# Performance work log

Hardware: AMD Instinct MI355X
Metric: run time of the kernel (lower is better)

Reference implementation:

```python
import jax, jax.numpy as jnp
import numpy as np

B, TV, TS, D = 16, 256, 32, 512


def setup_inputs() -> dict:
    key = jax.random.key(0)
    ks = jax.random.split(key, 8)
    return {
        "video_feature": jax.random.normal(ks[0], (B, TV, D), dtype=jnp.float32),
        "video_mask": jnp.ones((B, TV), dtype=jnp.float32),
        "sentence_feature": jax.random.normal(ks[1], (B, TS, D), dtype=jnp.float32),
        "sentence_mask": jnp.ones((B, TS), dtype=jnp.float32),
        "w1": jax.random.normal(ks[2], (D, D), dtype=jnp.float32) * (1.0 / np.sqrt(D)),
        "b1": jax.random.normal(ks[3], (D,), dtype=jnp.float32) * 0.02,
        "w2": jax.random.normal(ks[4], (D, D), dtype=jnp.float32) * (1.0 / np.sqrt(D)),
        "wt": jax.random.normal(ks[5], (D,), dtype=jnp.float32) * (1.0 / np.sqrt(D)),
    }


def reference(video_feature, video_mask, sentence_feature, sentence_mask, w1, b1, w2, wt):
    # tmp1: [B, Tv, D] masked video projection (Linear with bias)
    tmp1 = (jnp.einsum("bvd,ed->bve", video_feature, w1) + b1) * video_mask[:, :, None]
    # tmp2: [B, Ts, D] masked sentence projection (Linear, no bias)
    tmp2 = jnp.einsum("bsd,ed->bse", sentence_feature, w2) * sentence_mask[:, :, None]
    # pairwise mask: [B, Tv, Ts]
    pair_mask = video_mask[:, :, None] * sentence_mask[:, None, :]
    # broadcast-add -> [B, Tv, Ts, D], mask, tanh, reduce with wt -> [B, Tv, Ts]
    tmp = (tmp1[:, :, None, :] + tmp2[:, None, :, :]) * pair_mask[..., None]
    M = jnp.einsum("bvsd,d->bvs", jnp.tanh(tmp), wt)
    return M * pair_mask
```

## Files before the change

kernel.cpp:

```cpp
#include <hip/hip_runtime.h>

#define BB 16
#define TV 256
#define TS 32
#define DD 512

typedef float    floatx4  __attribute__((ext_vector_type(4)));
typedef short    short8   __attribute__((ext_vector_type(8)));
typedef unsigned short ushort8 __attribute__((ext_vector_type(8)));

static __device__ __forceinline__ unsigned short f2bf(float f) {
    unsigned int u = __float_as_uint(f);
    u += 0x7FFFu + ((u >> 16) & 1u);
    return (unsigned short)(u >> 16);
}

__global__ __launch_bounds__(256) void ta_convert(
    const float* __restrict__ video, const float* __restrict__ sent,
    const float* __restrict__ w1,    const float* __restrict__ w2,
    unsigned short* __restrict__ vb, unsigned short* __restrict__ sb,
    unsigned short* __restrict__ w1b, unsigned short* __restrict__ w2b)
{
    const int NV = BB * TV * DD, NS = BB * TS * DD, NW = DD * DD;
    const int base = (blockIdx.x * 256 + threadIdx.x) * 8;
    const float* src; unsigned short* dst; int off;
    if      (base < NV)           { src = video; dst = vb;  off = base; }
    else if (base < NV + NS)      { src = sent;  dst = sb;  off = base - NV; }
    else if (base < NV + NS + NW) { src = w1;    dst = w1b; off = base - NV - NS; }
    else                          { src = w2;    dst = w2b; off = base - NV - NS - NW; }
    const float4 a = *(const float4*)(src + off);
    const float4 b = *(const float4*)(src + off + 4);
    ushort8 o;
    o[0] = f2bf(a.x); o[1] = f2bf(a.y); o[2] = f2bf(a.z); o[3] = f2bf(a.w);
    o[4] = f2bf(b.x); o[5] = f2bf(b.y); o[6] = f2bf(b.z); o[7] = f2bf(b.w);
    *(ushort8*)(dst + off) = o;
}

__global__ __launch_bounds__(256) void ta_mfma_gemm(
    const unsigned short* __restrict__ vb, const unsigned short* __restrict__ w1b,
    const float* __restrict__ b1,          const float* __restrict__ vmask,
    float* __restrict__ tmp1,
    const unsigned short* __restrict__ sb, const unsigned short* __restrict__ w2b,
    const float* __restrict__ smask,       unsigned short* __restrict__ tmp2,
    const float* __restrict__ wt,          float* __restrict__ wsum)
{
    const int t = threadIdx.x;

    if (blockIdx.x == 0 && t < 64) {
        float v = 0.f;
        for (int i = t; i < DD; i += 64) v += wt[i];
        for (int off = 32; off; off >>= 1) v += __shfl_down(v, off);
        if (t == 0) wsum[0] = v;
    }

    const bool g2 = (blockIdx.x >= 512);
    const int bid = g2 ? (int)blockIdx.x - 512 : (int)blockIdx.x;
    const unsigned short* __restrict__ A  = g2 ? sb    : vb;
    const unsigned short* __restrict__ W  = g2 ? w2b   : w1b;
    const float* __restrict__ rm          = g2 ? smask : vmask;
    const int m0 = (bid >> 3) * 64;
    const int n0 = (bid & 7) * 64;

    __shared__ unsigned short As[64 * 64];
    __shared__ unsigned short Bs[64 * 64];

    const int lane = t & 63;
    const int wid  = t >> 6;
    const int wm   = wid >> 1, wn = wid & 1;
    const int lr   = lane & 15, kg = lane >> 4;

    const int row0 = t >> 3, c80 = t & 7;
    const int row1 = (t + 256) >> 3, c81 = t & 7;
    const int idx0 = row0 * 64 + ((c80 ^ (row0 & 7)) << 3);
    const int idx1 = row1 * 64 + ((c81 ^ (row1 & 7)) << 3);

    floatx4 acc[2][2] = {};

    for (int k0 = 0; k0 < DD; k0 += 64) {
        const ushort8 a0v = *(const ushort8*)&A[(size_t)(m0 + row0) * DD + k0 + c80 * 8];
        const ushort8 a1v = *(const ushort8*)&A[(size_t)(m0 + row1) * DD + k0 + c81 * 8];
        const ushort8 b0v = *(const ushort8*)&W[(size_t)(n0 + row0) * DD + k0 + c80 * 8];
        const ushort8 b1v = *(const ushort8*)&W[(size_t)(n0 + row1) * DD + k0 + c81 * 8];
        __syncthreads();
        *(ushort8*)&As[idx0] = a0v;
        *(ushort8*)&As[idx1] = a1v;
        *(ushort8*)&Bs[idx0] = b0v;
        *(ushort8*)&Bs[idx1] = b1v;
        __syncthreads();

#pragma unroll
        for (int kk = 0; kk < 2; ++kk) {
            const int kc = kk * 4 + kg;
            const int ml0 = wm * 32 + lr, ml1 = ml0 + 16;
            const int nl0 = wn * 32 + lr, nl1 = nl0 + 16;
            short8 a0 = *(const short8*)&As[ml0 * 64 + ((kc ^ (ml0 & 7)) << 3)];
            short8 a1 = *(const short8*)&As[ml1 * 64 + ((kc ^ (ml1 & 7)) << 3)];
            short8 b0 = *(const short8*)&Bs[nl0 * 64 + ((kc ^ (nl0 & 7)) << 3)];
            short8 b1 = *(const short8*)&Bs[nl1 * 64 + ((kc ^ (nl1 & 7)) << 3)];
            acc[0][0] = __builtin_amdgcn_mfma_f32_16x16x32_bf16(a0, b0, acc[0][0], 0, 0, 0);
            acc[0][1] = __builtin_amdgcn_mfma_f32_16x16x32_bf16(a0, b1, acc[0][1], 0, 0, 0);
            acc[1][0] = __builtin_amdgcn_mfma_f32_16x16x32_bf16(a1, b0, acc[1][0], 0, 0, 0);
            acc[1][1] = __builtin_amdgcn_mfma_f32_16x16x32_bf16(a1, b1, acc[1][1], 0, 0, 0);
        }
    }

#pragma unroll
    for (int fm = 0; fm < 2; ++fm)
#pragma unroll
        for (int fn = 0; fn < 2; ++fn)
#pragma unroll
            for (int r = 0; r < 4; ++r) {
                const int m = m0 + wm * 32 + fm * 16 + kg * 4 + r;
                const int n = n0 + wn * 32 + fn * 16 + lr;
                const float mk = rm[m];
                const float val = acc[fm][fn][r];
                if (!g2) tmp1[(size_t)m * DD + n] = (val + b1[n]) * mk;
                else     tmp2[(size_t)m * DD + n] = f2bf(val * mk);
            }
}

__global__ __launch_bounds__(512) void ta_tanh_main(
    const float* __restrict__ tmp1,
    const unsigned short* __restrict__ tmp2,
    const float* __restrict__ wt,
    const float* __restrict__ wsum,
    const float* __restrict__ vmask,
    const float* __restrict__ smask,
    float* __restrict__ out)
{
    __shared__ unsigned short t2s[TS * DD];
    __shared__ float part[512];

    const int t  = threadIdx.x;
    const int b  = blockIdx.x >> 6;
    const int v0 = (blockIdx.x & 63) << 2;

    {
        const unsigned short* src = tmp2 + (size_t)b * TS * DD;
#pragma unroll
        for (int i = 0; i < 4; ++i) {
            const int chunk = t + 512 * i;
            const int row = chunk >> 6;
            const int c   = chunk & 63;
            ushort8 val = *(const ushort8*)&src[chunk * 8];
            *(ushort8*)&t2s[row * DD + ((c ^ (row & 15)) << 3)] = val;
        }
    }
    __syncthreads();

    const int s  = t & 31;
    const int vi = (t >> 5) & 3;
    const int q  = __builtin_amdgcn_readfirstlane(t >> 7);
    const int v  = v0 + vi;

    const float pm = vmask[b * TV + v] * smask[b * TS + s];
    const float ce = pm * 2.885390082f;
    const float* __restrict__ x1p = tmp1 + ((size_t)(b * TV + v)) * DD + q * 128;
    const float* __restrict__ wtp = wt + q * 128;
    const int rowbase = s * DD;
    const int swz = s & 15;

    float acc0 = 0.f, acc1 = 0.f;
#pragma unroll 2
    for (int i = 0; i < 16; ++i) {
        ushort8 x2v = *(const ushort8*)&t2s[rowbase + (((q * 16 + i) ^ swz) << 3)];
        floatx4 x1a = *(const floatx4*)(x1p + i * 8);
        floatx4 x1b = *(const floatx4*)(x1p + i * 8 + 4);
#pragma unroll
        for (int j = 0; j < 4; ++j) {
            const float x2f = __uint_as_float((unsigned)x2v[j] << 16);
            const float e   = __builtin_amdgcn_exp2f((x1a[j] + x2f) * ce);
            acc0 = fmaf(wtp[i * 8 + j], __builtin_amdgcn_rcpf(e + 1.f), acc0);
        }
#pragma unroll
        for (int j = 0; j < 4; ++j) {
            const float x2f = __uint_as_float((unsigned)x2v[j + 4] << 16);
            const float e   = __builtin_amdgcn_exp2f((x1b[j] + x2f) * ce);
            acc1 = fmaf(wtp[i * 8 + j + 4], __builtin_amdgcn_rcpf(e + 1.f), acc1);
        }
    }

    part[t] = acc0 + acc1;
    __syncthreads();

    if (t < 128) {
        const float sum = part[t] + part[t + 128] + part[t + 256] + part[t + 384];
        const int s2 = t & 31, vi2 = t >> 5;
        const int v2 = v0 + vi2;
        const float pm2 = vmask[b * TV + v2] * smask[b * TS + s2];
        out[((size_t)b * TV + v2) * TS + s2] = pm2 * (wsum[0] - 2.f * sum);
    }
}

extern "C" void kernel_launch(void* const* d_in, const int* in_sizes, int n_in,
                              void* d_out, int out_size, void* d_ws, size_t ws_size,
                              hipStream_t stream)
{
    const float* video = (const float*)d_in[0];
    const float* vmask = (const float*)d_in[1];
    const float* sent  = (const float*)d_in[2];
    const float* smask = (const float*)d_in[3];
    const float* w1    = (const float*)d_in[4];
    const float* b1    = (const float*)d_in[5];
    const float* w2    = (const float*)d_in[6];
    const float* wt    = (const float*)d_in[7];
    float* out = (float*)d_out;

    const size_t NV = (size_t)BB * TV * DD, NS = (size_t)BB * TS * DD, NW = (size_t)DD * DD;

    float* tmp1          = (float*)d_ws;
    unsigned short* tmp2 = (unsigned short*)(tmp1 + NV);
    float* wsum          = (float*)(tmp2 + NS);
    unsigned short* vb   = (unsigned short*)(wsum + 4);
    unsigned short* sb   = vb + NV;
    unsigned short* w1b  = sb + NS;
    unsigned short* w2b  = w1b + NW;

    const int total8 = (int)((NV + NS + 2 * NW) / 8);
    ta_convert<<<dim3(total8 / 256), dim3(256), 0, stream>>>(
        video, sent, w1, w2, vb, sb, w1b, w2b);
    ta_mfma_gemm<<<dim3(512 + 64), dim3(256), 0, stream>>>(
        vb, w1b, b1, vmask, tmp1, sb, w2b, smask, tmp2, wt, wsum);
    ta_tanh_main<<<dim3(BB * (TV / 4)), dim3(512), 0, stream>>>(
        tmp1, tmp2, wt, wsum, vmask, smask, out);
}
```

Measured before the change: 42.58 us.

## Store tmp1 in bf16 and double-buffer GEMM with direct global-to-LDS loads

```diff
diff --git a/kernel.cpp b/kernel.cpp
--- a/kernel.cpp
+++ b/kernel.cpp
@@ -39,7 +39,7 @@
 __global__ __launch_bounds__(256) void ta_mfma_gemm(
     const unsigned short* __restrict__ vb, const unsigned short* __restrict__ w1b,
     const float* __restrict__ b1,          const float* __restrict__ vmask,
-    float* __restrict__ tmp1,
+    unsigned short* __restrict__ tmp1,
     const unsigned short* __restrict__ sb, const unsigned short* __restrict__ w2b,
     const float* __restrict__ smask,       unsigned short* __restrict__ tmp2,
     const float* __restrict__ wt,          float* __restrict__ wsum)
@@ -55,54 +55,74 @@
 
     const bool g2 = (blockIdx.x >= 512);
     const int bid = g2 ? (int)blockIdx.x - 512 : (int)blockIdx.x;
-    const unsigned short* __restrict__ A  = g2 ? sb    : vb;
-    const unsigned short* __restrict__ W  = g2 ? w2b   : w1b;
-    const float* __restrict__ rm          = g2 ? smask : vmask;
-    const int m0 = (bid >> 3) * 64;
-    const int n0 = (bid & 7) * 64;
-
-    __shared__ unsigned short As[64 * 64];
-    __shared__ unsigned short Bs[64 * 64];
+    const unsigned short* __restrict__ A = g2 ? sb    : vb;
+    const unsigned short* __restrict__ W = g2 ? w2b   : w1b;
+    const float* __restrict__ rm         = g2 ? smask : vmask;
+    const int m0 = (g2 ? (bid & 7)  : (bid & 63)) * 64;
+    const int n0 = (g2 ? (bid >> 3) : (bid >> 6)) * 64;
+
+    __shared__ unsigned short As[2][4096];
+    __shared__ unsigned short Bs[2][4096];
 
     const int lane = t & 63;
     const int wid  = t >> 6;
     const int wm   = wid >> 1, wn = wid & 1;
     const int lr   = lane & 15, kg = lane >> 4;
 
-    const int row0 = t >> 3, c80 = t & 7;
-    const int row1 = (t + 256) >> 3, c81 = t & 7;
-    const int idx0 = row0 * 64 + ((c80 ^ (row0 & 7)) << 3);
-    const int idx1 = row1 * 64 + ((c81 ^ (row1 & 7)) << 3);
+    const int r0 = t >> 3,          g0c = (t & 7) ^ (r0 & 7);
+    const int r1 = (t + 256) >> 3,  g1c = (t & 7) ^ (r1 & 7);
+    const unsigned short* a0p = A + (size_t)(m0 + r0) * DD + g0c * 8;
+    const unsigned short* a1p = A + (size_t)(m0 + r1) * DD + g1c * 8;
+    const unsigned short* w0p = W + (size_t)(n0 + r0) * DD + g0c * 8;
+    const unsigned short* w1p = W + (size_t)(n0 + r1) * DD + g1c * 8;
+    const int l0 = t * 8;
+    const int l1 = (t + 256) * 8;
+
+#define TA_STAGE(buf, koff) do {                                               \
+    __builtin_amdgcn_global_load_lds(                                          \
+        (const __attribute__((address_space(1))) void*)(a0p + (koff)),         \
+        (__attribute__((address_space(3))) void*)&As[buf][l0], 16, 0, 0);      \
+    __builtin_amdgcn_global_load_lds(                                          \
+        (const __attribute__((address_space(1))) void*)(a1p + (koff)),         \
+        (__attribute__((address_space(3))) void*)&As[buf][l1], 16, 0, 0);      \
+    __builtin_amdgcn_global_load_lds(                                          \
+        (const __attribute__((address_space(1))) void*)(w0p + (koff)),         \
+        (__attribute__((address_space(3))) void*)&Bs[buf][l0], 16, 0, 0);      \
+    __builtin_amdgcn_global_load_lds(                                          \
+        (const __attribute__((address_space(1))) void*)(w1p + (koff)),         \
+        (__attribute__((address_space(3))) void*)&Bs[buf][l1], 16, 0, 0);      \
+  } while (0)
 
     floatx4 acc[2][2] = {};
 
-    for (int k0 = 0; k0 < DD; k0 += 64) {
-        const ushort8 a0v = *(const ushort8*)&A[(size_t)(m0 + row0) * DD + k0 + c80 * 8];
-        const ushort8 a1v = *(const ushort8*)&A[(size_t)(m0 + row1) * DD + k0 + c81 * 8];
-        const ushort8 b0v = *(const ushort8*)&W[(size_t)(n0 + row0) * DD + k0 + c80 * 8];
-        const ushort8 b1v = *(const ushort8*)&W[(size_t)(n0 + row1) * DD + k0 + c81 * 8];
-        __syncthreads();
-        *(ushort8*)&As[idx0] = a0v;
-        *(ushort8*)&As[idx1] = a1v;
-        *(ushort8*)&Bs[idx0] = b0v;
-        *(ushort8*)&Bs[idx1] = b1v;
-        __syncthreads();
-
+    const int ml0 = wm * 32 + lr, ml1 = ml0 + 16;
+    const int nl0 = wn * 32 + lr, nl1 = nl0 + 16;
+    const int sa0 = ml0 * 64, sa1 = ml1 * 64;
+    const int sb0 = nl0 * 64, sb1 = nl1 * 64;
+    const int xa = ml0 & 7, xb = nl0 & 7;
+
+    TA_STAGE(0, 0);
+    __syncthreads();
+
+    int cur = 0;
+    for (int step = 0; step < 8; ++step) {
+        if (step < 7) TA_STAGE(cur ^ 1, (step + 1) * 64);
 #pragma unroll
         for (int kk = 0; kk < 2; ++kk) {
             const int kc = kk * 4 + kg;
-            const int ml0 = wm * 32 + lr, ml1 = ml0 + 16;
-            const int nl0 = wn * 32 + lr, nl1 = nl0 + 16;
-            short8 a0 = *(const short8*)&As[ml0 * 64 + ((kc ^ (ml0 & 7)) << 3)];
-            short8 a1 = *(const short8*)&As[ml1 * 64 + ((kc ^ (ml1 & 7)) << 3)];
-            short8 b0 = *(const short8*)&Bs[nl0 * 64 + ((kc ^ (nl0 & 7)) << 3)];
-            short8 b1 = *(const short8*)&Bs[nl1 * 64 + ((kc ^ (nl1 & 7)) << 3)];
+            short8 a0 = *(const short8*)&As[cur][sa0 + ((kc ^ xa) << 3)];
+            short8 a1 = *(const short8*)&As[cur][sa1 + ((kc ^ xa) << 3)];
+            short8 b0 = *(const short8*)&Bs[cur][sb0 + ((kc ^ xb) << 3)];
+            short8 b1 = *(const short8*)&Bs[cur][sb1 + ((kc ^ xb) << 3)];
             acc[0][0] = __builtin_amdgcn_mfma_f32_16x16x32_bf16(a0, b0, acc[0][0], 0, 0, 0);
             acc[0][1] = __builtin_amdgcn_mfma_f32_16x16x32_bf16(a0, b1, acc[0][1], 0, 0, 0);
             acc[1][0] = __builtin_amdgcn_mfma_f32_16x16x32_bf16(a1, b0, acc[1][0], 0, 0, 0);
             acc[1][1] = __builtin_amdgcn_mfma_f32_16x16x32_bf16(a1, b1, acc[1][1], 0, 0, 0);
         }
-    }
+        __syncthreads();
+        cur ^= 1;
+    }
+#undef TA_STAGE
 
 #pragma unroll
     for (int fm = 0; fm < 2; ++fm)
@@ -114,13 +134,13 @@
                 const int n = n0 + wn * 32 + fn * 16 + lr;
                 const float mk = rm[m];
                 const float val = acc[fm][fn][r];
-                if (!g2) tmp1[(size_t)m * DD + n] = (val + b1[n]) * mk;
+                if (!g2) tmp1[(size_t)m * DD + n] = f2bf((val + b1[n]) * mk);
                 else     tmp2[(size_t)m * DD + n] = f2bf(val * mk);
             }
 }
 
 __global__ __launch_bounds__(512) void ta_tanh_main(
-    const float* __restrict__ tmp1,
+    const unsigned short* __restrict__ tmp1,
     const unsigned short* __restrict__ tmp2,
     const float* __restrict__ wt,
     const float* __restrict__ wsum,
@@ -155,28 +175,28 @@
 
     const float pm = vmask[b * TV + v] * smask[b * TS + s];
     const float ce = pm * 2.885390082f;
-    const float* __restrict__ x1p = tmp1 + ((size_t)(b * TV + v)) * DD + q * 128;
+    const unsigned short* __restrict__ x1p = tmp1 + ((size_t)(b * TV + v)) * DD + q * 128;
     const float* __restrict__ wtp = wt + q * 128;
     const int rowbase = s * DD;
     const int swz = s & 15;
 
     float acc0 = 0.f, acc1 = 0.f;
-#pragma unroll 2
     for (int i = 0; i < 16; ++i) {
         ushort8 x2v = *(const ushort8*)&t2s[rowbase + (((q * 16 + i) ^ swz) << 3)];
-        floatx4 x1a = *(const floatx4*)(x1p + i * 8);
-        floatx4 x1b = *(const floatx4*)(x1p + i * 8 + 4);
+        ushort8 x1v = *(const ushort8*)&x1p[i * 8];
 #pragma unroll
         for (int j = 0; j < 4; ++j) {
+            const float x1f = __uint_as_float((unsigned)x1v[j] << 16);
             const float x2f = __uint_as_float((unsigned)x2v[j] << 16);
-            const float e   = __builtin_amdgcn_exp2f((x1a[j] + x2f) * ce);
+            const float e   = __builtin_amdgcn_exp2f((x1f + x2f) * ce);
             acc0 = fmaf(wtp[i * 8 + j], __builtin_amdgcn_rcpf(e + 1.f), acc0);
         }
 #pragma unroll
-        for (int j = 0; j < 4; ++j) {
-            const float x2f = __uint_as_float((unsigned)x2v[j + 4] << 16);
-            const float e   = __builtin_amdgcn_exp2f((x1b[j] + x2f) * ce);
-            acc1 = fmaf(wtp[i * 8 + j + 4], __builtin_amdgcn_rcpf(e + 1.f), acc1);
+        for (int j = 4; j < 8; ++j) {
+            const float x1f = __uint_as_float((unsigned)x1v[j] << 16);
+            const float x2f = __uint_as_float((unsigned)x2v[j] << 16);
+            const float e   = __builtin_amdgcn_exp2f((x1f + x2f) * ce);
+            acc1 = fmaf(wtp[i * 8 + j], __builtin_amdgcn_rcpf(e + 1.f), acc1);
         }
     }
 
@@ -208,13 +228,13 @@
 
     const size_t NV = (size_t)BB * TV * DD, NS = (size_t)BB * TS * DD, NW = (size_t)DD * DD;
 
-    float* tmp1          = (float*)d_ws;
-    unsigned short* tmp2 = (unsigned short*)(tmp1 + NV);
-    float* wsum          = (float*)(tmp2 + NS);
-    unsigned short* vb   = (unsigned short*)(wsum + 4);
+    unsigned short* tmp1 = (unsigned short*)d_ws;
+    unsigned short* tmp2 = tmp1 + NV;
+    unsigned short* vb   = tmp2 + NS;
     unsigned short* sb   = vb + NV;
     unsigned short* w1b  = sb + NS;
     unsigned short* w2b  = w1b + NW;
+    float* wsum          = (float*)(w2b + NW);
 
     const int total8 = (int)((NV + NS + 2 * NW) / 8);
     ta_convert<<<dim3(total8 / 256), dim3(256), 0, stream>>>(
```

After: 41.91 us. Within noise of the previous version (-1.6%).
